# Optimization experiments

Hardware: AMD Instinct MI355X
Metric: run time of the kernel (lower is better)

The kernel has to match this reference:

```python
import jax, jax.numpy as jnp
import numpy as np
import math

B, S, DIN = 8, 2048, 64
D, G, OUT_SEQ = 64, 5, 512
LN_EPS = 1e-5


def setup_inputs() -> dict:
    key = jax.random.key(0)
    ks = jax.random.split(key, 4)
    seq = jax.random.normal(ks[0], (B, S, DIN), dtype=jnp.float32)
    M = jax.random.uniform(ks[1], (D, DIN), minval=-0.5, maxval=0.5, dtype=jnp.float32)
    P = jax.random.uniform(ks[2], (D, D, G), minval=-0.1, maxval=0.1, dtype=jnp.float32)
    Linker = jax.random.uniform(ks[3], (S, OUT_SEQ), minval=-0.1, maxval=0.1, dtype=jnp.float32)
    ln_gamma = jnp.ones((D,), dtype=jnp.float32)
    ln_beta = jnp.zeros((D,), dtype=jnp.float32)
    return {"seq": seq, "M": M, "P": P, "Linker": Linker, "ln_gamma": ln_gamma, "ln_beta": ln_beta}


def _layer_norm(x, gamma, beta):
    mu = jnp.mean(x, axis=-1, keepdims=True)
    var = jnp.mean(jnp.square(x - mu), axis=-1, keepdims=True)
    return (x - mu) * jax.lax.rsqrt(var + LN_EPS) * gamma + beta


def reference(seq, M, P, Linker, ln_gamma, ln_beta):
    # periods[i,j,g] = i*(D*G) + j*G + g + 2 (constant buffer)
    periods = (jnp.arange(D * D * G, dtype=jnp.float32) + 2.0).reshape(D, D, G)
    k = jnp.arange(S, dtype=jnp.float32)
    # phi: (S, D, D, G) cosine basis
    phi = jnp.cos(2.0 * math.pi * k[:, None, None, None] / periods)
    # Precontract basis: W[k,i,j] = sum_g P[i,j,g] * phi[k,i,j,g]  -> (S, D, D)
    W = jnp.einsum('kijg,ijg->kij', phi, P)

    Z0 = jnp.einsum('bsd,od->bso', seq, M)          # x @ M^T, (B,S,D)
    Z = _layer_norm(Z0, ln_gamma, ln_beta)          # (B,S,D)
    # T[b,k,i] = sum_j Z[b,k,j] * W[k,i,j]
    T = jnp.einsum('bkj,kij->bki', Z, W)            # (B,S,D)
    U = jnp.einsum('bki,ko->boi', T, Linker)        # (B,OUT_SEQ,D)
    # shared residual: (x @ M^T)^T @ Linker, using pre-LayerNorm projection
    residual = jnp.einsum('bki,ko->boi', Z0, Linker)
    return U + residual
```

## Files before the change

### kernel.cpp

```cpp
#include <hip/hip_runtime.h>
#include <math.h>

#define SS 2048
#define OSQ 512
#define GG 5

typedef unsigned short u16;
typedef unsigned int u32;
typedef __attribute__((ext_vector_type(8))) short s16x8;
typedef __attribute__((ext_vector_type(4))) float v4f;
typedef __attribute__((ext_vector_type(16))) float v16f;

__device__ __forceinline__ float rcp_f(float x) {
    float r; asm("v_rcp_f32 %0, %1" : "=v"(r) : "v"(x)); return r;
}
__device__ __forceinline__ float cos_rev(float x) {
    float fr, c;
    asm("v_fract_f32 %0, %1" : "=v"(fr) : "v"(x));
    asm("v_cos_f32 %0, %1" : "=v"(c) : "v"(fr));
    return c;
}
__device__ __forceinline__ float cos01(float x) {
    float c; asm("v_cos_f32 %0, %1" : "=v"(c) : "v"(x)); return c;
}
__device__ __forceinline__ u16 f2bf(float f) {
    u32 u = __float_as_uint(f);
    return (u16)((u + 0x7FFFu + ((u >> 16) & 1u)) >> 16);
}
__device__ __forceinline__ float bf2f(u16 h) {
    return __uint_as_float((u32)h << 16);
}
__device__ __forceinline__ void gload16(const void* g, void* l) {
    __builtin_amdgcn_global_load_lds((const __attribute__((address_space(1))) void*)g,
                                     (__attribute__((address_space(3))) void*)l, 16, 0, 0);
}


__global__ __launch_bounds__(512, 1) void kF(const float* __restrict__ seq,
                                             const float* __restrict__ Mm,
                                             const float* __restrict__ P,
                                             const float* __restrict__ gamma,
                                             const float* __restrict__ beta,
                                             const float* __restrict__ Lnk,
                                             u16* __restrict__ Lt,
                                             u16* __restrict__ Vt) {
    __shared__ __align__(16) u16 SEQb[64 * 64];
    __shared__ __align__(16) u16 Mb[64 * 64];
    __shared__ __align__(16) u16 SZb[64 * 64];
    __shared__ float Z0l[64 * 68];
    __shared__ u32 Ta32[8 * 2 * 64 * 5];

    const int t = threadIdx.x;

    if (blockIdx.x < 128) {
        const int tb = blockIdx.x;
        const int k0t = (tb & 15) * 128;
        const int o0 = (tb >> 4) * 64;
        const int og = o0 + (t & 63);
        const int sp2 = (t >> 6) * 2;
        #pragma unroll
        for (int ss2 = 0; ss2 < 2; ++ss2) {
            const int s = sp2 + ss2;
            float v[8];
            #pragma unroll
            for (int j = 0; j < 8; ++j)
                v[j] = Lnk[(size_t)(k0t + s * 8 + j) * OSQ + og];
            uint4 pk;
            pk.x = (u32)f2bf(v[0]) | ((u32)f2bf(v[1]) << 16);
            pk.y = (u32)f2bf(v[2]) | ((u32)f2bf(v[3]) << 16);
            pk.z = (u32)f2bf(v[4]) | ((u32)f2bf(v[5]) << 16);
            pk.w = (u32)f2bf(v[6]) | ((u32)f2bf(v[7]) << 16);
            size_t idx16 = ((size_t)(og >> 5) * 128 + ((k0t + s * 8) >> 4)) * 64
                         + (og & 31) + 32 * (s & 1);
            *(uint4*)&Lt[idx16 * 8] = pk;
        }
        return;
    }

    const int bidA = blockIdx.x - 128;
    const int l = t & 63;
    const int w = t >> 6;
    const int k0 = bidA * 8;
    const float kf0 = (float)k0;

    const int h = w >> 2;
    const int i0 = (w & 3) * 16;
    const int i_w = i0 + (l & 15);
    const int jc_w = h * 4 + (l >> 4);

    float pr[40];
    {
        const float4* P4 = (const float4*)(P + ((size_t)i_w * 64 + jc_w * 8) * 5);
        #pragma unroll
        for (int q = 0; q < 10; ++q) {
            float4 v = P4[q];
            pr[q * 4 + 0] = v.x; pr[q * 4 + 1] = v.y; pr[q * 4 + 2] = v.z; pr[q * 4 + 3] = v.w;
        }
    }

    {
        int row = t >> 3, ch = t & 7;
        int b = row >> 3, kq = row & 7;
        const float* sp = &seq[((size_t)b * SS + k0 + kq) * 64 + ch * 8];
        float4 a = *(const float4*)sp, bb4 = *(const float4*)(sp + 4);
        uint4 pk;
        pk.x = (u32)f2bf(a.x) | ((u32)f2bf(a.y) << 16);
        pk.y = (u32)f2bf(a.z) | ((u32)f2bf(a.w) << 16);
        pk.z = (u32)f2bf(bb4.x) | ((u32)f2bf(bb4.y) << 16);
        pk.w = (u32)f2bf(bb4.z) | ((u32)f2bf(bb4.w) << 16);
        *(uint4*)&SEQb[row * 64 + ((ch ^ (row & 7)) * 8)] = pk;

        const float* mp = &Mm[(size_t)row * 64 + ch * 8];
        float4 c = *(const float4*)mp, d = *(const float4*)(mp + 4);
        uint4 pm;
        pm.x = (u32)f2bf(c.x) | ((u32)f2bf(c.y) << 16);
        pm.y = (u32)f2bf(c.z) | ((u32)f2bf(c.w) << 16);
        pm.z = (u32)f2bf(d.x) | ((u32)f2bf(d.y) << 16);
        pm.w = (u32)f2bf(d.z) | ((u32)f2bf(d.w) << 16);
        *(uint4*)&Mb[row * 64 + ((ch ^ (row & 7)) * 8)] = pm;
    }

    float c0[40], c1[40], t2c[40];
    #pragma unroll
    for (int m = 0; m < 8; ++m) {
        #pragma unroll
        for (int g = 0; g < GG; ++g) {
            int idx = m * 5 + g;
            float pf = (float)((i_w * 64 + jc_w * 8 + m) * 5 + g + 2);
            float inv = rcp_f(pf);
            c0[idx] = cos_rev(kf0 * inv);
            c1[idx] = cos_rev((kf0 + 1.0f) * inv);
            float ct = cos01(inv);
            t2c[idx] = ct + ct;
        }
    }

    float gm[8], bt[8];
    {
        int oc = t & 7;
        float4 a = *(const float4*)&gamma[oc * 8], b = *(const float4*)&gamma[oc * 8 + 4];
        float4 c = *(const float4*)&beta[oc * 8],  d = *(const float4*)&beta[oc * 8 + 4];
        gm[0]=a.x; gm[1]=a.y; gm[2]=a.z; gm[3]=a.w; gm[4]=b.x; gm[5]=b.y; gm[6]=b.z; gm[7]=b.w;
        bt[0]=c.x; bt[1]=c.y; bt[2]=c.z; bt[3]=c.w; bt[4]=d.x; bt[5]=d.y; bt[6]=d.z; bt[7]=d.w;
    }
    __syncthreads();

    if (w < 4) {
        const int qr = w & 1, qc = w >> 1;
        v16f acc = {0,0,0,0,0,0,0,0,0,0,0,0,0,0,0,0};
        const int rowA = qr * 32 + (l & 31);
        const int rowB = qc * 32 + (l & 31);
        #pragma unroll
        for (int ks = 0; ks < 4; ++ks) {
            int cA = (ks * 2 + (l >> 5)) ^ (rowA & 7);
            int cB = (ks * 2 + (l >> 5)) ^ (rowB & 7);
            s16x8 af = *(const s16x8*)&SEQb[rowA * 64 + cA * 8];
            s16x8 bf = *(const s16x8*)&Mb[rowB * 64 + cB * 8];
            acc = __builtin_amdgcn_mfma_f32_32x32x16_bf16(af, bf, acc, 0, 0, 0);
        }
        #pragma unroll
        for (int q = 0; q < 16; ++q) {
            int row = qr * 32 + (q & 3) + 8 * (q >> 2) + 4 * (l >> 5);
            int col = qc * 32 + (l & 31);
            Z0l[row * 68 + col] = acc[q];
        }
    }
    __syncthreads();

    {
        const int rI = t >> 3, oc = t & 7;
        float z0v[8];
        float4 a = *(const float4*)&Z0l[rI * 68 + oc * 8];
        float4 b = *(const float4*)&Z0l[rI * 68 + oc * 8 + 4];
        z0v[0]=a.x; z0v[1]=a.y; z0v[2]=a.z; z0v[3]=a.w; z0v[4]=b.x; z0v[5]=b.y; z0v[6]=b.z; z0v[7]=b.w;
        float s1 = ((z0v[0]+z0v[1])+(z0v[2]+z0v[3])) + ((z0v[4]+z0v[5])+(z0v[6]+z0v[7]));
        s1 += __shfl_xor(s1, 1); s1 += __shfl_xor(s1, 2); s1 += __shfl_xor(s1, 4);
        float mu = s1 * 0.015625f;
        float sq = 0.f;
        #pragma unroll
        for (int m = 0; m < 8; ++m) { float dv = z0v[m] - mu; sq = fmaf(dv, dv, sq); }
        sq += __shfl_xor(sq, 1); sq += __shfl_xor(sq, 2); sq += __shfl_xor(sq, 4);
        float rstd = rsqrtf(sq * 0.015625f + 1e-5f);
        u16 zb[8];
        #pragma unroll
        for (int m = 0; m < 8; ++m)
            zb[m] = f2bf(fmaf((z0v[m] - mu) * rstd, gm[m], bt[m]));
        uint4 pk;
        pk.x = (u32)zb[0] | ((u32)zb[1] << 16);
        pk.y = (u32)zb[2] | ((u32)zb[3] << 16);
        pk.z = (u32)zb[4] | ((u32)zb[5] << 16);
        pk.w = (u32)zb[6] | ((u32)zb[7] << 16);
        int slot = oc ^ ((rI >> 3) & 7);
        *(uint4*)&SZb[rI * 64 + slot * 8] = pk;
    }
    __syncthreads();

    const int bcl = l & 7;
    #pragma unroll
    for (int kc = 0; kc < 8; ++kc) {
        if (kc >= 2) {
            #pragma unroll
            for (int x = 0; x < 40; ++x) {
                float cn = fmaf(t2c[x], c1[x], -c0[x]);
                c0[x] = c1[x]; c1[x] = cn;
            }
        }
        s16x8 bw;
        #pragma unroll
        for (int j = 0; j < 8; ++j) {
            float a = 0.f;
            #pragma unroll
            for (int g = 0; g < GG; ++g) {
                float ph = (kc == 0) ? c0[j * 5 + g] : c1[j * 5 + g];
                a = fmaf(pr[j * 5 + g], ph, a);
            }
            bw[j] = (short)f2bf(a);
        }
        int arow = bcl * 8 + kc;
        int slot = (h * 4 + (l >> 4)) ^ bcl;
        s16x8 az = *(const s16x8*)&SZb[arow * 64 + slot * 8];
        v4f zc = {0.f, 0.f, 0.f, 0.f};
        v4f d = __builtin_amdgcn_mfma_f32_16x16x32_bf16(az, bw, zc, 0, 0, 0);
        if (l < 32) {
            int ii = i0 + (l & 15);
            int bb2 = (l >> 4) * 2;
            u32 base = (u32)((kc * 2 + h) * 64 + ii) * 5 + bb2;
            Ta32[base]     = (u32)f2bf(d[0]) | ((u32)f2bf(d[1]) << 16);
            Ta32[base + 1] = (u32)f2bf(d[2]) | ((u32)f2bf(d[3]) << 16);
        }
    }
    __syncthreads();

    {
        const u16* TaR = (const u16*)Ta32;
        float vk[8];
        #pragma unroll
        for (int kc = 0; kc < 8; ++kc)
            vk[kc] = bf2f(TaR[((kc * 2 + 0) * 64 + l) * 10 + w])
                   + bf2f(TaR[((kc * 2 + 1) * 64 + l) * 10 + w])
                   + Z0l[(w * 8 + kc) * 68 + l];
        uint4 pk;
        pk.x = (u32)f2bf(vk[0]) | ((u32)f2bf(vk[1]) << 16);
        pk.y = (u32)f2bf(vk[2]) | ((u32)f2bf(vk[3]) << 16);
        pk.z = (u32)f2bf(vk[4]) | ((u32)f2bf(vk[5]) << 16);
        pk.w = (u32)f2bf(vk[6]) | ((u32)f2bf(vk[7]) << 16);
        const int ks = k0 >> 4;
        const int hi = (k0 >> 3) & 1;
        size_t idx16 = ((size_t)(w * 2 + (l >> 5)) * 128 + ks) * 64 + (l & 31) + 32 * hi;
        *(uint4*)&Vt[idx16 * 8] = pk;
    }
}

__global__ __launch_bounds__(256, 2) void kB2(const u16* __restrict__ Lt,
                                              const u16* __restrict__ Vt,
                                              float* __restrict__ out) {
    __shared__ __align__(16) u16 LB[4][2][2][2048];
    const int t = threadIdx.x;
    const int l = t & 63, w = t >> 6;
    const int bid = blockIdx.x;
    const int it = bid & 1, ot = (bid >> 1) & 15, b = bid >> 5;

    const u16* aG = Lt + (((size_t)ot * 128 + w * 32) * 64 + l) * 8;
    const u16* bG = Vt + (((size_t)(b * 2 + it) * 128 + w * 32) * 64 + l) * 8;

    v16f acc0 = {0,0,0,0,0,0,0,0,0,0,0,0,0,0,0,0};
    v16f acc1 = acc0;

#define STAGE(c, buf)                                                          \
    {                                                                          \
        _Pragma("unroll")                                                      \
        for (int ksl = 0; ksl < 4; ++ksl) {                                    \
            gload16(aG + ((c) * 4 + ksl) * 512, &LB[w][buf][0][ksl * 512]);    \
            gload16(bG + ((c) * 4 + ksl) * 512, &LB[w][buf][1][ksl * 512]);    \
        }                                                                      \
    }

    STAGE(0, 0);
    STAGE(1, 1);
    #pragma unroll
    for (int c = 0; c < 8; ++c) {
        if (c < 7) { asm volatile("s_waitcnt vmcnt(8)" ::: "memory"); }
        else       { asm volatile("s_waitcnt vmcnt(0)" ::: "memory"); }
        __builtin_amdgcn_sched_barrier(0);
        const int buf = c & 1;
        #pragma unroll
        for (int ksl = 0; ksl < 4; ++ksl) {
            s16x8 A = *(const s16x8*)&LB[w][buf][0][ksl * 512 + l * 8];
            s16x8 B = *(const s16x8*)&LB[w][buf][1][ksl * 512 + l * 8];
            if (ksl & 1) acc1 = __builtin_amdgcn_mfma_f32_32x32x16_bf16(A, B, acc1, 0, 0, 0);
            else         acc0 = __builtin_amdgcn_mfma_f32_32x32x16_bf16(A, B, acc0, 0, 0, 0);
        }
        asm volatile("s_waitcnt lgkmcnt(0)" ::: "memory");
        __builtin_amdgcn_sched_barrier(0);
        if (c + 2 < 8) STAGE(c + 2, buf);
    }
#undef STAGE

    __syncthreads();
    float* red = (float*)LB;
    {
        const int base = (w * 64 + l) * 17;
        #pragma unroll
        for (int r = 0; r < 16; ++r) red[base + r] = acc0[r] + acc1[r];
    }
    __syncthreads();
    {
        const int icol = t & 31;
        const int ob = (t >> 5) * 4;
        #pragma unroll
        for (int q = 0; q < 4; ++q) {
            const int orow = ob + q;
            const int hi = (orow >> 2) & 1;
            const int r = (orow & 3) | ((orow >> 3) << 2);
            const int lp = icol + 32 * hi;
            float s = red[(0 * 64 + lp) * 17 + r] + red[(1 * 64 + lp) * 17 + r]
                    + red[(2 * 64 + lp) * 17 + r] + red[(3 * 64 + lp) * 17 + r];
            out[((size_t)b * OSQ + ot * 32 + orow) * 64 + it * 32 + icol] = s;
        }
    }
}

extern "C" void kernel_launch(void* const* d_in, const int* in_sizes, int n_in,
                              void* d_out, int out_size, void* d_ws, size_t ws_size,
                              hipStream_t stream) {
    const float* seq   = (const float*)d_in[0];
    const float* Mm    = (const float*)d_in[1];
    const float* P     = (const float*)d_in[2];
    const float* Lnk   = (const float*)d_in[3];
    const float* gamma = (const float*)d_in[4];
    const float* beta  = (const float*)d_in[5];

    u16* Lt = (u16*)d_ws;
    u16* Vt = (u16*)((char*)d_ws + (2u << 20));

    kF<<<384, 512, 0, stream>>>(seq, Mm, P, gamma, beta, Lnk, Lt, Vt);
    kB2<<<256, 256, 0, stream>>>(Lt, Vt, (float*)d_out);
}
```

Baseline: 21.43 us.

## Load GEMM operands directly to registers and remap block order in kB2

Drops the LDS double-buffered global_load_lds staging in the second GEMM kernel and has each wave load its MFMA fragments straight from global memory into registers, relying on the fully unrolled loop to keep loads in flight. It also remaps the block index so that consecutive blocks are spread across batches and tiles, which is meant to improve L2 locality across the device's XCDs. This removes LDS round trips and waitcnt synchronisation but depends on the compiler to schedule the loads for latency hiding, and it raises register pressure.

```diff
diff --git a/kernel.cpp b/kernel.cpp
--- a/kernel.cpp
+++ b/kernel.cpp
@@ -29,10 +29,6 @@
 }
 __device__ __forceinline__ float bf2f(u16 h) {
     return __uint_as_float((u32)h << 16);
-}
-__device__ __forceinline__ void gload16(const void* g, void* l) {
-    __builtin_amdgcn_global_load_lds((const __attribute__((address_space(1))) void*)g,
-                                     (__attribute__((address_space(3))) void*)l, 16, 0, 0);
 }
 
 
@@ -254,11 +250,12 @@
 __global__ __launch_bounds__(256, 2) void kB2(const u16* __restrict__ Lt,
                                               const u16* __restrict__ Vt,
                                               float* __restrict__ out) {
-    __shared__ __align__(16) u16 LB[4][2][2][2048];
+    __shared__ float red[4 * 64 * 17];
     const int t = threadIdx.x;
     const int l = t & 63, w = t >> 6;
-    const int bid = blockIdx.x;
-    const int it = bid & 1, ot = (bid >> 1) & 15, b = bid >> 5;
+    const int p = blockIdx.x;
+    const int lg = (p & 7) * 32 + (p >> 3);
+    const int it = lg & 1, ot = (lg >> 1) & 15, b = lg >> 5;
 
     const u16* aG = Lt + (((size_t)ot * 128 + w * 32) * 64 + l) * 8;
     const u16* bG = Vt + (((size_t)(b * 2 + it) * 128 + w * 32) * 64 + l) * 8;
@@ -266,38 +263,14 @@
     v16f acc0 = {0,0,0,0,0,0,0,0,0,0,0,0,0,0,0,0};
     v16f acc1 = acc0;
 
-#define STAGE(c, buf)                                                          \
-    {                                                                          \
-        _Pragma("unroll")                                                      \
-        for (int ksl = 0; ksl < 4; ++ksl) {                                    \
-            gload16(aG + ((c) * 4 + ksl) * 512, &LB[w][buf][0][ksl * 512]);    \
-            gload16(bG + ((c) * 4 + ksl) * 512, &LB[w][buf][1][ksl * 512]);    \
-        }                                                                      \
-    }
-
-    STAGE(0, 0);
-    STAGE(1, 1);
     #pragma unroll
-    for (int c = 0; c < 8; ++c) {
-        if (c < 7) { asm volatile("s_waitcnt vmcnt(8)" ::: "memory"); }
-        else       { asm volatile("s_waitcnt vmcnt(0)" ::: "memory"); }
-        __builtin_amdgcn_sched_barrier(0);
-        const int buf = c & 1;
-        #pragma unroll
-        for (int ksl = 0; ksl < 4; ++ksl) {
-            s16x8 A = *(const s16x8*)&LB[w][buf][0][ksl * 512 + l * 8];
-            s16x8 B = *(const s16x8*)&LB[w][buf][1][ksl * 512 + l * 8];
-            if (ksl & 1) acc1 = __builtin_amdgcn_mfma_f32_32x32x16_bf16(A, B, acc1, 0, 0, 0);
-            else         acc0 = __builtin_amdgcn_mfma_f32_32x32x16_bf16(A, B, acc0, 0, 0, 0);
-        }
-        asm volatile("s_waitcnt lgkmcnt(0)" ::: "memory");
-        __builtin_amdgcn_sched_barrier(0);
-        if (c + 2 < 8) STAGE(c + 2, buf);
-    }
-#undef STAGE
-
-    __syncthreads();
-    float* red = (float*)LB;
+    for (int ks = 0; ks < 32; ++ks) {
+        s16x8 A = *(const s16x8*)(aG + ks * 512);
+        s16x8 B = *(const s16x8*)(bG + ks * 512);
+        if (ks & 1) acc1 = __builtin_amdgcn_mfma_f32_32x32x16_bf16(A, B, acc1, 0, 0, 0);
+        else        acc0 = __builtin_amdgcn_mfma_f32_32x32x16_bf16(A, B, acc0, 0, 0, 0);
+    }
+
     {
         const int base = (w * 64 + l) * 17;
         #pragma unroll
```

After: 27.35 us. 1.28x slower.

## Fold Linker bf16 transpose into main kF blocks and remap kB2 block order

Applied to the files above, without the earlier changes.

Removes the 128 dedicated blocks that converted Linker to bf16 tiles. Each of the remaining 256 kF blocks now loads its own 8 Linker rows early, alongside the other work, and writes the packed tile at the end. kB2 block indices are permuted so that consecutive blocks spread across batches and output tiles, presumably to balance the load across XCDs and improve cache locality. The cost is more registers held in kF and somewhat more work in the critical-path blocks.

```diff
diff --git a/kernel.cpp b/kernel.cpp
--- a/kernel.cpp
+++ b/kernel.cpp
@@ -51,36 +51,9 @@
     __shared__ u32 Ta32[8 * 2 * 64 * 5];
 
     const int t = threadIdx.x;
-
-    if (blockIdx.x < 128) {
-        const int tb = blockIdx.x;
-        const int k0t = (tb & 15) * 128;
-        const int o0 = (tb >> 4) * 64;
-        const int og = o0 + (t & 63);
-        const int sp2 = (t >> 6) * 2;
-        #pragma unroll
-        for (int ss2 = 0; ss2 < 2; ++ss2) {
-            const int s = sp2 + ss2;
-            float v[8];
-            #pragma unroll
-            for (int j = 0; j < 8; ++j)
-                v[j] = Lnk[(size_t)(k0t + s * 8 + j) * OSQ + og];
-            uint4 pk;
-            pk.x = (u32)f2bf(v[0]) | ((u32)f2bf(v[1]) << 16);
-            pk.y = (u32)f2bf(v[2]) | ((u32)f2bf(v[3]) << 16);
-            pk.z = (u32)f2bf(v[4]) | ((u32)f2bf(v[5]) << 16);
-            pk.w = (u32)f2bf(v[6]) | ((u32)f2bf(v[7]) << 16);
-            size_t idx16 = ((size_t)(og >> 5) * 128 + ((k0t + s * 8) >> 4)) * 64
-                         + (og & 31) + 32 * (s & 1);
-            *(uint4*)&Lt[idx16 * 8] = pk;
-        }
-        return;
-    }
-
-    const int bidA = blockIdx.x - 128;
     const int l = t & 63;
     const int w = t >> 6;
-    const int k0 = bidA * 8;
+    const int k0 = blockIdx.x * 8;
     const float kf0 = (float)k0;
 
     const int h = w >> 2;
@@ -97,6 +70,11 @@
             pr[q * 4 + 0] = v.x; pr[q * 4 + 1] = v.y; pr[q * 4 + 2] = v.z; pr[q * 4 + 3] = v.w;
         }
     }
+
+    float lnv[8];
+    #pragma unroll
+    for (int j = 0; j < 8; ++j)
+        lnv[j] = Lnk[(size_t)(k0 + j) * OSQ + t];
 
     {
         int row = t >> 3, ch = t & 7;
@@ -249,6 +227,18 @@
         size_t idx16 = ((size_t)(w * 2 + (l >> 5)) * 128 + ks) * 64 + (l & 31) + 32 * hi;
         *(uint4*)&Vt[idx16 * 8] = pk;
     }
+
+    {
+        uint4 pk;
+        pk.x = (u32)f2bf(lnv[0]) | ((u32)f2bf(lnv[1]) << 16);
+        pk.y = (u32)f2bf(lnv[2]) | ((u32)f2bf(lnv[3]) << 16);
+        pk.z = (u32)f2bf(lnv[4]) | ((u32)f2bf(lnv[5]) << 16);
+        pk.w = (u32)f2bf(lnv[6]) | ((u32)f2bf(lnv[7]) << 16);
+        const int ks = k0 >> 4;
+        const int hi = (k0 >> 3) & 1;
+        size_t idx16 = ((size_t)(t >> 5) * 128 + ks) * 64 + (t & 31) + 32 * hi;
+        *(uint4*)&Lt[idx16 * 8] = pk;
+    }
 }
 
 __global__ __launch_bounds__(256, 2) void kB2(const u16* __restrict__ Lt,
@@ -257,8 +247,9 @@
     __shared__ __align__(16) u16 LB[4][2][2][2048];
     const int t = threadIdx.x;
     const int l = t & 63, w = t >> 6;
-    const int bid = blockIdx.x;
-    const int it = bid & 1, ot = (bid >> 1) & 15, b = bid >> 5;
+    const int p = blockIdx.x;
+    const int lg = (p & 7) * 32 + (p >> 3);
+    const int it = lg & 1, ot = (lg >> 1) & 15, b = lg >> 5;
 
     const u16* aG = Lt + (((size_t)ot * 128 + w * 32) * 64 + l) * 8;
     const u16* bG = Vt + (((size_t)(b * 2 + it) * 128 + w * 32) * 64 + l) * 8;
@@ -333,6 +324,6 @@
     u16* Lt = (u16*)d_ws;
     u16* Vt = (u16*)((char*)d_ws + (2u << 20));
 
-    kF<<<384, 512, 0, stream>>>(seq, Mm, P, gamma, beta, Lnk, Lt, Vt);
+    kF<<<256, 512, 0, stream>>>(seq, Mm, P, gamma, beta, Lnk, Lt, Vt);
     kB2<<<256, 256, 0, stream>>>(Lt, Vt, (float*)d_out);
 }
```

New measurement: 21.67 us. No clear change (+1.1%).
